# Kernel optimization log

Hardware: AMD Instinct MI355X
Metric: run time of the kernel (lower is better)

Reference implementation:

```python
import jax, jax.numpy as jnp
import numpy as np

N = 30000   # total nodes
E = 240000  # edges
B = 64      # graphs / proteins
H = 10      # GATv2 heads
C = 78      # per-head out dim (= xd_features)
D = H * C   # 780
SEQ = 1000
EMB = 128
LH = 64     # LSTM hidden per direction


def _lstm_dir(xs, Wih, Whh, bih, bhh, reverse):
    # xs: [T, Bn, EMB]; PyTorch gate order i,f,g,o
    Bn = xs.shape[1]
    h0 = jnp.zeros((Bn, LH), xs.dtype)
    def step(carry, xt):
        h, c = carry
        z = xt @ Wih.T + h @ Whh.T + bih + bhh
        i, f, g, o = jnp.split(z, 4, axis=-1)
        c = jax.nn.sigmoid(f) * c + jax.nn.sigmoid(i) * jnp.tanh(g)
        h = jax.nn.sigmoid(o) * jnp.tanh(c)
        return (h, c), h
    _, hs = jax.lax.scan(step, (h0, h0), xs, reverse=reverse)
    return hs


def setup_inputs() -> dict:
    k = jax.random.key(0)
    nxt = lambda i: jax.random.fold_in(k, i)
    s = 0.05
    d = {}
    d['x'] = jax.random.normal(nxt(0), (N, C), jnp.float32)
    d['edge_index'] = jax.random.randint(nxt(1), (2, E), 0, N)
    d['batch'] = jnp.sort(jax.random.randint(nxt(2), (N,), 0, B))
    d['target'] = jax.random.randint(nxt(3), (B, SEQ), 0, 26)
    # GATv2Conv params (share_weights=False)
    d['Wl'] = jax.random.normal(nxt(4), (C, D), jnp.float32) * s
    d['Wr'] = jax.random.normal(nxt(5), (C, D), jnp.float32) * s
    d['att'] = jax.random.normal(nxt(6), (H, C), jnp.float32) * s
    d['gat_b'] = jnp.zeros((D,), jnp.float32)
    # GCNConv params
    d['gcn_w'] = jax.random.normal(nxt(7), (D, D), jnp.float32) * s
    d['gcn_b'] = jnp.zeros((D,), jnp.float32)
    # protein branch
    d['emb'] = jax.random.normal(nxt(8), (26, EMB), jnp.float32) * s
    for tag, base in (('f', 9), ('b', 13)):
        d['Wih_' + tag] = jax.random.normal(nxt(base), (4 * LH, EMB), jnp.float32) * s
        d['Whh_' + tag] = jax.random.normal(nxt(base + 1), (4 * LH, LH), jnp.float32) * s
        d['bih_' + tag] = jnp.zeros((4 * LH,), jnp.float32)
        d['bhh_' + tag] = jnp.zeros((4 * LH,), jnp.float32)
    d['conv_w'] = jax.random.normal(nxt(17), (32, SEQ, 8), jnp.float32) * s
    d['conv_b'] = jnp.zeros((32,), jnp.float32)
    d['fcp_w'] = jax.random.normal(nxt(18), (32 * 121, 128), jnp.float32) * s
    d['fcp_b'] = jnp.zeros((128,), jnp.float32)
    # combined MLP (actual concat dim = 2*780 + 128 = 1688)
    d['fc1_w'] = jax.random.normal(nxt(19), (1688, 1024), jnp.float32) * s
    d['fc1_b'] = jnp.zeros((1024,), jnp.float32)
    d['fc2_w'] = jax.random.normal(nxt(20), (1024, 512), jnp.float32) * s
    d['fc2_b'] = jnp.zeros((512,), jnp.float32)
    d['out_w'] = jax.random.normal(nxt(21), (512, 1), jnp.float32) * s
    d['out_b'] = jnp.zeros((1,), jnp.float32)
    return d


def reference(x, edge_index, batch, target, Wl, Wr, att, gat_b, gcn_w, gcn_b,
              emb, Wih_f, Whh_f, bih_f, bhh_f, Wih_b, Whh_b, bih_b, bhh_b,
              conv_w, conv_b, fcp_w, fcp_b, fc1_w, fc1_b, fc2_w, fc2_b,
              out_w, out_b):
    # ---- graph branch (eval mode: dropout off) ----
    loops = jnp.arange(N)
    src = jnp.concatenate([edge_index[0], loops])  # self loops (PyG default)
    dst = jnp.concatenate([edge_index[1], loops])

    # GATv2Conv
    xl = (x @ Wl).reshape(N, H, C)
    xr = (x @ Wr).reshape(N, H, C)
    e = jax.nn.leaky_relu(xl[src] + xr[dst], 0.2)       # [E+N, H, C]
    logit = jnp.einsum('ehc,hc->eh', e, att)            # [E+N, H]
    m = jax.ops.segment_max(logit, dst, num_segments=N)
    ex = jnp.exp(logit - m[dst])
    den = jax.ops.segment_sum(ex, dst, num_segments=N)
    alpha = ex / den[dst]
    h = jax.ops.segment_sum(alpha[:, :, None] * xl[src], dst, num_segments=N)
    h = jax.nn.elu(h.reshape(N, D) + gat_b)

    # GCNConv with symmetric normalization
    hw = h @ gcn_w
    deg = jax.ops.segment_sum(jnp.ones_like(src, jnp.float32), dst, num_segments=N)
    dinv = jnp.where(deg > 0, jax.lax.rsqrt(jnp.maximum(deg, 1e-12)), 0.0)
    norm = dinv[src] * dinv[dst]
    g = jax.ops.segment_sum(norm[:, None] * hw[src], dst, num_segments=N) + gcn_b
    g = jax.nn.relu(g)

    # global max + mean pooling per graph
    gmax = jax.ops.segment_max(g, batch, num_segments=B)
    cnt = jax.ops.segment_sum(jnp.ones((N,), jnp.float32), batch, num_segments=B)
    gmean = jax.ops.segment_sum(g, batch, num_segments=B) / jnp.maximum(cnt, 1.0)[:, None]
    graph_feat = jnp.concatenate([gmax, gmean], axis=1)  # [B, 1560]

    # ---- protein branch ----
    et = emb[target]                                     # [B, SEQ, EMB]
    # nn.LSTM default batch_first=False: time axis is axis 0 (=B), batch axis is SEQ
    hf = _lstm_dir(et, Wih_f, Whh_f, bih_f, bhh_f, reverse=False)
    hb = _lstm_dir(et, Wih_b, Whh_b, bih_b, bhh_b, reverse=True)
    hcat = jnp.concatenate([hf, hb], axis=-1)            # [B, SEQ, 128]
    conv = jax.lax.conv_general_dilated(hcat, conv_w, (1,), 'VALID',
                                        dimension_numbers=('NCH', 'OIH', 'NCH'))
    conv = conv + conv_b[None, :, None]                  # [B, 32, 121]
    prot = conv.reshape(B, 32 * 121) @ fcp_w + fcp_b     # [B, 128]

    # ---- combined head ----
    comb = jnp.concatenate([graph_feat, prot], axis=1)   # [B, 1688]
    h1 = jax.nn.relu(comb @ fc1_w + fc1_b)
    h2 = jax.nn.relu(h1 @ fc2_w + fc2_b)
    return h2 @ out_w + out_b                            # [B, 1]
```

## Files before the change

kernel.cpp:

```cpp
#include <hip/hip_runtime.h>
#include <hip/hip_bf16.h>
#include <math.h>

static constexpr int NN   = 30000;
static constexpr int EE   = 240000;
static constexpr int ET   = EE + NN;
static constexpr int BB   = 64;
static constexpr int HH   = 10;
static constexpr int CC   = 78;
static constexpr int CCP  = 80;
static constexpr int DD   = HH * CC;
static constexpr int DDP  = HH * CCP;
static constexpr int NNP  = 30080;
static constexpr int KXP  = 96;
static constexpr int NBP  = 896;
static constexpr int SEQ  = 1000;
static constexpr int EMB  = 128;
static constexpr int LH   = 64;
static constexpr int COMBD = 2 * DD + 128;
static constexpr int PCHUNK = 64;
static constexpr int USL  = CCP / 2;
static constexpr size_t SLICE_U = (size_t)NNP * USL;

typedef __attribute__((ext_vector_type(8))) short short8;
typedef __attribute__((ext_vector_type(4))) float f32x4;

__device__ __forceinline__ float bflo(unsigned int u) {
    return __uint_as_float(u << 16);
}
__device__ __forceinline__ float bfhi(unsigned int u) {
    return __uint_as_float(u & 0xffff0000u);
}
__device__ __forceinline__ unsigned int pack2bf(float x, float y) {
    __hip_bfloat16 bx = __float2bfloat16(x), by = __float2bfloat16(y);
    unsigned short ux = *reinterpret_cast<unsigned short*>(&bx);
    unsigned short uy = *reinterpret_cast<unsigned short*>(&by);
    return (unsigned int)ux | ((unsigned int)uy << 16);
}
__device__ __forceinline__ float fast_sigmoid(float x) {
    return __builtin_amdgcn_rcpf(1.f + __expf(-x));
}
__device__ __forceinline__ float fast_tanh(float x) {
    float e = __expf(2.f * x);
    return 1.f - 2.f * __builtin_amdgcn_rcpf(e + 1.f);
}
__device__ __forceinline__ void glds16(const unsigned short* g, unsigned short* l) {
    __builtin_amdgcn_global_load_lds(
        (const __attribute__((address_space(1))) unsigned int*)g,
        (__attribute__((address_space(3))) unsigned int*)l, 16, 0, 0);
}

__global__ __launch_bounds__(256) void gemm_glds_sl(const __hip_bfloat16* __restrict__ A,
                                                    const __hip_bfloat16* __restrict__ Bt,
                                                    __hip_bfloat16* __restrict__ C,
                                                    int M, int N, int Kp) {
    __shared__ unsigned short As[128 * 32];
    __shared__ unsigned short Bs[128 * 32];
    const int tid  = threadIdx.x;
    const int lane = tid & 63, wid = tid >> 6;
    const int wr = wid >> 1, wc = wid & 1;
    const int l15 = lane & 15, l4 = lane >> 4;
    int l = blockIdx.y * gridDim.x + blockIdx.x;
    {
        int nwg = gridDim.x * gridDim.y;
        int q = nwg >> 3, r = nwg & 7;
        int xcd = l & 7, idx = l >> 3;
        l = (xcd < r) ? (xcd * (q + 1) + idx) : (r * (q + 1) + (xcd - r) * q + idx);
    }
    const int bm = (l / gridDim.x) * 128;
    const int bn = (l % gridDim.x) * 128;
    const unsigned short* Au = (const unsigned short*)A;
    const unsigned short* Bu = (const unsigned short*)Bt;
    const int lrow = lane >> 2, lseg = (lane & 3) * 8;

    f32x4 acc[4][4];
#pragma unroll
    for (int m = 0; m < 4; ++m)
#pragma unroll
        for (int n = 0; n < 4; ++n) acc[m][n] = (f32x4){0.f, 0.f, 0.f, 0.f};

    for (int k0 = 0; k0 < Kp; k0 += 32) {
#pragma unroll
        for (int c = 0; c < 2; ++c) {
            int rbase = wid * 32 + c * 16;
            glds16(Au + (size_t)(bm + rbase + lrow) * Kp + k0 + lseg, &As[rbase * 32]);
            glds16(Bu + (size_t)(bn + rbase + lrow) * Kp + k0 + lseg, &Bs[rbase * 32]);
        }
        __syncthreads();
        short8 a[4], b[4];
#pragma unroll
        for (int m = 0; m < 4; ++m)
            a[m] = *reinterpret_cast<const short8*>(&As[(wr * 64 + m * 16 + l15) * 32 + l4 * 8]);
#pragma unroll
        for (int n = 0; n < 4; ++n)
            b[n] = *reinterpret_cast<const short8*>(&Bs[(wc * 64 + n * 16 + l15) * 32 + l4 * 8]);
#pragma unroll
        for (int m = 0; m < 4; ++m)
#pragma unroll
            for (int n = 0; n < 4; ++n)
                acc[m][n] = __builtin_amdgcn_mfma_f32_16x16x32_bf16(a[m], b[n], acc[m][n], 0, 0, 0);
        __syncthreads();
    }
#pragma unroll
    for (int m = 0; m < 4; ++m)
#pragma unroll
        for (int n = 0; n < 4; ++n)
#pragma unroll
            for (int r = 0; r < 4; ++r) {
                int row = bm + wr * 64 + m * 16 + l4 * 4 + r;
                int col = bn + wc * 64 + n * 16 + l15;
                if (row < M && col < N) {
                    int sl = col / CC, c = col % CC;
                    C[(size_t)sl * NNP * CCP + (size_t)row * CCP + c] =
                        __float2bfloat16(acc[m][n][r]);
                }
            }
}

__global__ __launch_bounds__(256) void gemm_bf16_mfma(const __hip_bfloat16* __restrict__ A,
                                                      const __hip_bfloat16* __restrict__ Bt,
                                                      float* __restrict__ C,
                                                      int M, int N, int K, int ldc) {
    constexpr int LDS_S = 40;
    __shared__ unsigned short As[128 * LDS_S];
    __shared__ unsigned short Bs[128 * LDS_S];
    const int tid  = threadIdx.x;
    const int lane = tid & 63, wid = tid >> 6;
    const int wr = wid >> 1, wc = wid & 1;
    const int l15 = lane & 15, l4 = lane >> 4;
    int l = blockIdx.y * gridDim.x + blockIdx.x;
    {
        int nwg = gridDim.x * gridDim.y;
        int q = nwg >> 3, r = nwg & 7;
        int xcd = l & 7, idx = l >> 3;
        l = (xcd < r) ? (xcd * (q + 1) + idx) : (r * (q + 1) + (xcd - r) * q + idx);
    }
    const int bm = (l / gridDim.x) * 128;
    const int bn = (l % gridDim.x) * 128;
    const int tr = tid >> 2, tc = (tid & 3) * 8;

    const unsigned short* Au = (const unsigned short*)A;
    const unsigned short* Bu = (const unsigned short*)Bt;

    f32x4 acc[4][4];
#pragma unroll
    for (int m = 0; m < 4; ++m)
#pragma unroll
        for (int n = 0; n < 4; ++n) acc[m][n] = (f32x4){0.f, 0.f, 0.f, 0.f};

    for (int k0 = 0; k0 < K; k0 += 32) {
#pragma unroll
        for (int half = 0; half < 2; ++half) {
            int row = tr + half * 64;
            {
                int grow = bm + row;
                short8 sv;
                if (grow < M && k0 + tc + 8 <= K) {
                    const unsigned int* p = (const unsigned int*)(Au + (size_t)grow * K + k0 + tc);
#pragma unroll
                    for (int j = 0; j < 4; ++j) {
                        unsigned int u = p[j];
                        sv[2 * j]     = (short)(u & 0xffffu);
                        sv[2 * j + 1] = (short)(u >> 16);
                    }
                } else {
#pragma unroll
                    for (int j = 0; j < 8; ++j) {
                        int gk = k0 + tc + j;
                        sv[j] = (grow < M && gk < K) ? (short)Au[(size_t)grow * K + gk] : (short)0;
                    }
                }
                *reinterpret_cast<short8*>(&As[row * LDS_S + tc]) = sv;
            }
            {
                int grow = bn + row;
                short8 sv;
                if (grow < N && k0 + tc + 8 <= K) {
                    const unsigned int* p = (const unsigned int*)(Bu + (size_t)grow * K + k0 + tc);
#pragma unroll
                    for (int j = 0; j < 4; ++j) {
                        unsigned int u = p[j];
                        sv[2 * j]     = (short)(u & 0xffffu);
                        sv[2 * j + 1] = (short)(u >> 16);
                    }
                } else {
#pragma unroll
                    for (int j = 0; j < 8; ++j) {
                        int gk = k0 + tc + j;
                        sv[j] = (grow < N && gk < K) ? (short)Bu[(size_t)grow * K + gk] : (short)0;
                    }
                }
                *reinterpret_cast<short8*>(&Bs[row * LDS_S + tc]) = sv;
            }
        }
        __syncthreads();
        short8 a[4], b[4];
#pragma unroll
        for (int m = 0; m < 4; ++m)
            a[m] = *reinterpret_cast<const short8*>(&As[(wr * 64 + m * 16 + l15) * LDS_S + l4 * 8]);
#pragma unroll
        for (int n = 0; n < 4; ++n)
            b[n] = *reinterpret_cast<const short8*>(&Bs[(wc * 64 + n * 16 + l15) * LDS_S + l4 * 8]);
#pragma unroll
        for (int m = 0; m < 4; ++m)
#pragma unroll
            for (int n = 0; n < 4; ++n)
                acc[m][n] = __builtin_amdgcn_mfma_f32_16x16x32_bf16(a[m], b[n], acc[m][n], 0, 0, 0);
        __syncthreads();
    }
#pragma unroll
    for (int m = 0; m < 4; ++m)
#pragma unroll
        for (int n = 0; n < 4; ++n)
#pragma unroll
            for (int r = 0; r < 4; ++r) {
                int row = bm + wr * 64 + m * 16 + l4 * 4 + r;
                int col = bn + wc * 64 + n * 16 + l15;
                if (row < M && col < N)
                    C[(size_t)row * ldc + col] = acc[m][n][r];
            }
}

__global__ void pad_x(const float* __restrict__ x, __hip_bfloat16* __restrict__ xp) {
    int idx = blockIdx.x * blockDim.x + threadIdx.x;
    if (idx >= NNP * KXP) return;
    int r = idx / KXP, c = idx % KXP;
    float v = (r < NN && c < CC) ? x[(size_t)r * CC + c] : 0.f;
    xp[idx] = __float2bfloat16(v);
}

__global__ void pad_wT(const float* __restrict__ w, __hip_bfloat16* __restrict__ wt) {
    int idx = blockIdx.x * blockDim.x + threadIdx.x;
    if (idx >= NBP * KXP) return;
    int n = idx / KXP, k = idx % KXP;
    float v = (n < DD && k < CC) ? w[(size_t)k * DD + n] : 0.f;
    wt[idx] = __float2bfloat16(v);
}

__global__ void pad_gcwT(const float* __restrict__ w, __hip_bfloat16* __restrict__ wt) {
    int idx = blockIdx.x * blockDim.x + threadIdx.x;
    if (idx >= NBP * DDP) return;
    int n = idx / DDP, kp = idx % DDP;
    int kc = kp % CCP;
    int k = (kp / CCP) * CC + kc;
    float v = (n < DD && kc < CC) ? w[(size_t)k * DD + n] : 0.f;
    wt[idx] = __float2bfloat16(v);
}

__global__ void transpose_f32(const float* __restrict__ in, float* __restrict__ out,
                              int Kdim, int Ndim) {
    int idx = blockIdx.x * blockDim.x + threadIdx.x;
    if (idx >= Kdim * Ndim) return;
    int n = idx / Kdim, k = idx % Kdim;
    out[idx] = in[(size_t)k * Ndim + n];
}

__global__ void pad_att(const float* __restrict__ att, float* __restrict__ att_p) {
    int idx = blockIdx.x * blockDim.x + threadIdx.x;
    if (idx >= HH * CCP) return;
    int h = idx / CCP, c = idx % CCP;
    att_p[idx] = (c < CC) ? att[h * CC + c] : 0.f;
}

__global__ void zero_pads(unsigned int* __restrict__ a, unsigned int* __restrict__ b) {
    int idx = blockIdx.x * blockDim.x + threadIdx.x;
    if (idx >= NN * HH) return;
    int n = idx / HH, h = idx % HH;
    size_t p = (size_t)h * SLICE_U + (size_t)n * USL + (USL - 1);
    a[p] = 0u;
    b[p] = 0u;
}

template <int ACT>
__global__ __launch_bounds__(256) void gemm_skinny(const float* __restrict__ A,
                                                   const float* __restrict__ Bt,
                                                   const float* __restrict__ bias,
                                                   float* __restrict__ C,
                                                   int M, int N, int K, int ldc) {
    int oidx = blockIdx.x * 4 + (threadIdx.x >> 6);
    int lane = threadIdx.x & 63;
    if (oidx >= M * N) return;
    int row = oidx / N, col = oidx % N;
    const float4* a = (const float4*)(A + (size_t)row * K);
    const float4* b = (const float4*)(Bt + (size_t)col * K);
    int K4 = K >> 2;
    float s = 0.f;
    for (int i = lane; i < K4; i += 64) {
        float4 x = a[i], y = b[i];
        s += x.x * y.x + x.y * y.y + x.z * y.z + x.w * y.w;
    }
#pragma unroll
    for (int off = 32; off; off >>= 1) s += __shfl_xor(s, off);
    if (lane == 0) {
        s += bias[col];
        if (ACT == 1) s = fmaxf(s, 0.f);
        C[(size_t)row * ldc + col] = s;
    }
}

__global__ void deg_count(const int* __restrict__ ei, int* __restrict__ deg) {
    int e = blockIdx.x * blockDim.x + threadIdx.x;
    if (e >= ET) return;
    int d = (e < EE) ? ei[EE + e] : (e - EE);
    atomicAdd(&deg[d], 1);
}

__global__ __launch_bounds__(1024) void scan_kernel(const int* __restrict__ deg,
                                                    int* __restrict__ offs) {
    __shared__ int lds[1024];
    int tid = threadIdx.x;
    const int chunk = (NN + 1023) / 1024;
    int base = tid * chunk;
    int s = 0;
    for (int i = 0; i < chunk; ++i) {
        int idx = base + i;
        if (idx < NN) s += deg[idx];
    }
    lds[tid] = s;
    __syncthreads();
    for (int d = 1; d < 1024; d <<= 1) {
        int v = (tid >= d) ? lds[tid - d] : 0;
        __syncthreads();
        lds[tid] += v;
        __syncthreads();
    }
    int run = (tid == 0) ? 0 : lds[tid - 1];
    for (int i = 0; i < chunk; ++i) {
        int idx = base + i;
        if (idx < NN) { offs[idx] = run; run += deg[idx]; }
    }
    if (tid == 1023) offs[NN] = lds[1023];
}

__global__ void csr_fill(const int* __restrict__ ei, const int* __restrict__ offs,
                         int* __restrict__ cursor, int* __restrict__ csr_src,
                         int* __restrict__ csr_dst) {
    int e = blockIdx.x * blockDim.x + threadIdx.x;
    if (e >= ET) return;
    int s = (e < EE) ? ei[e] : (e - EE);
    int d = (e < EE) ? ei[EE + e] : (e - EE);
    int pos = atomicAdd(&cursor[d], 1);
    int slot = offs[d] + pos;
    csr_src[slot] = s;
    csr_dst[slot] = d;
}

__global__ void dinv_kernel(const int* __restrict__ deg, float* __restrict__ dinv) {
    int n = blockIdx.x * blockDim.x + threadIdx.x;
    if (n >= NN) return;
    float dg = (float)deg[n];
    dinv[n] = (dg > 0.f) ? 1.f / sqrtf(dg) : 0.f;
}

__device__ __forceinline__ float dot2lr(unsigned int a, unsigned int b, float w0, float w1) {
    float v0 = bflo(a) + bflo(b);
    float v1 = bfhi(a) + bfhi(b);
    v0 = (v0 > 0.f) ? v0 : 0.2f * v0;
    v1 = (v1 > 0.f) ? v1 : 0.2f * v1;
    return w0 * v0 + w1 * v1;
}

__global__ void gat_logits(const unsigned short* __restrict__ xl_sl,
                           const unsigned short* __restrict__ xr_sl,
                           const float* __restrict__ att_p, const int* __restrict__ csr_src,
                           const int* __restrict__ csr_dst, float* __restrict__ logit_hm) {
    int i = blockIdx.x * blockDim.x + threadIdx.x;
    int h = blockIdx.y;
    if (i >= ET) return;
    int s = csr_src[i], d = csr_dst[i];
    const uint4* pl = (const uint4*)(xl_sl + (size_t)h * NNP * CCP + (size_t)s * CCP);
    const uint4* pr = (const uint4*)(xr_sl + (size_t)h * NNP * CCP + (size_t)d * CCP);
    const float* pa = att_p + h * CCP;
    float acc = 0.f;
#pragma unroll
    for (int q = 0; q < CCP / 8; ++q) {
        uint4 a = pl[q], b = pr[q];
        const float* p8 = pa + q * 8;
        acc += dot2lr(a.x, b.x, p8[0], p8[1]);
        acc += dot2lr(a.y, b.y, p8[2], p8[3]);
        acc += dot2lr(a.z, b.z, p8[4], p8[5]);
        acc += dot2lr(a.w, b.w, p8[6], p8[7]);
    }
    logit_hm[(size_t)h * ET + i] = acc;
}

__global__ void gat_softmax(const int* __restrict__ offs, float* __restrict__ logit_hm) {
    int idx = blockIdx.x * blockDim.x + threadIdx.x;
    if (idx >= NN * HH) return;
    int n = idx / HH, h = idx % HH;
    int i0 = offs[n], i1 = offs[n + 1];
    float* lg = logit_hm + (size_t)h * ET;
    float m = -1e30f;
    for (int i = i0; i < i1; ++i) m = fmaxf(m, lg[i]);
    float den = 0.f;
    for (int i = i0; i < i1; ++i) {
        float e = __expf(lg[i] - m);
        lg[i] = e;
        den += e;
    }
    float inv = __builtin_amdgcn_rcpf(den);
    for (int i = i0; i < i1; ++i) lg[i] *= inv;
}

__global__ __launch_bounds__(256) void gat_aggregate(const int* __restrict__ offs,
                                                     const int* __restrict__ csr_src,
                                                     const float* __restrict__ alpha_hm,
                                                     const unsigned int* __restrict__ xl_sl,
                                                     const float* __restrict__ gat_b,
                                                     unsigned int* __restrict__ hout) {
    int n = blockIdx.x;
    int tid = threadIdx.x;
    int i0 = offs[n], i1 = offs[n + 1];
    const int U = DDP / 2;
    int u0 = tid, u1 = tid + 256;
    bool v1 = (u1 < U);
    int h0 = u0 / USL, c0 = u0 % USL;
    int h1 = v1 ? u1 / USL : 0, c1 = v1 ? u1 % USL : 0;
    const unsigned int* s0 = xl_sl + (size_t)h0 * SLICE_U + c0;
    const unsigned int* s1 = xl_sl + (size_t)h1 * SLICE_U + c1;
    const float* a0p = alpha_hm + (size_t)h0 * ET;
    const float* a1p = alpha_hm + (size_t)h1 * ET;
    float lo0 = 0.f, hi0 = 0.f, lo1 = 0.f, hi1 = 0.f;
    for (int i = i0; i < i1; ++i) {
        int src = csr_src[i];
        unsigned int w0 = s0[(size_t)src * USL];
        float p0 = a0p[i];
        lo0 += p0 * bflo(w0);
        hi0 += p0 * bfhi(w0);
        if (v1) {
            unsigned int w1 = s1[(size_t)src * USL];
            float p1 = a1p[i];
            lo1 += p1 * bflo(w1);
            hi1 += p1 * bfhi(w1);
        }
    }
    unsigned int ov0 = 0u, ov1 = 0u;
    if (c0 != USL - 1) {
        int d = h0 * CC + 2 * c0;
        float x = lo0 + gat_b[d];     x = (x > 0.f) ? x : __expf(x) - 1.f;
        float y = hi0 + gat_b[d + 1]; y = (y > 0.f) ? y : __expf(y) - 1.f;
        ov0 = pack2bf(x, y);
    }
    hout[(size_t)n * U + u0] = ov0;
    if (v1) {
        if (c1 != USL - 1) {
            int d = h1 * CC + 2 * c1;
            float x = lo1 + gat_b[d];     x = (x > 0.f) ? x : __expf(x) - 1.f;
            float y = hi1 + gat_b[d + 1]; y = (y > 0.f) ? y : __expf(y) - 1.f;
            ov1 = pack2bf(x, y);
        }
        hout[(size_t)n * U + u1] = ov1;
    }
}

__global__ __launch_bounds__(256) void gcn_aggregate(const int* __restrict__ offs,
                                                     const int* __restrict__ csr_src,
                                                     const float* __restrict__ dinv,
                                                     const unsigned int* __restrict__ hw_sl,
                                                     const float* __restrict__ gcn_b,
                                                     unsigned int* __restrict__ g_sl) {
    int n = blockIdx.x;
    int tid = threadIdx.x;
    float din = dinv[n];
    int i0 = offs[n], i1 = offs[n + 1];
    const int U = DDP / 2;
    int u0 = tid, u1 = tid + 256;
    bool v1 = (u1 < U);
    int h0 = u0 / USL, c0 = u0 % USL;
    int h1 = v1 ? u1 / USL : 0, c1 = v1 ? u1 % USL : 0;
    const unsigned int* s0 = hw_sl + (size_t)h0 * SLICE_U + c0;
    const unsigned int* s1 = hw_sl + (size_t)h1 * SLICE_U + c1;
    float lo0 = 0.f, hi0 = 0.f, lo1 = 0.f, hi1 = 0.f;
    for (int i = i0; i < i1; ++i) {
        int src = csr_src[i];
        float w = dinv[src] * din;
        unsigned int w0 = s0[(size_t)src * USL];
        lo0 += w * bflo(w0);
        hi0 += w * bfhi(w0);
        if (v1) {
            unsigned int w1 = s1[(size_t)src * USL];
            lo1 += w * bflo(w1);
            hi1 += w * bfhi(w1);
        }
    }
    if (c0 != USL - 1) {
        int d = h0 * CC + 2 * c0;
        float x = fmaxf(lo0 + gcn_b[d], 0.f);
        float y = fmaxf(hi0 + gcn_b[d + 1], 0.f);
        g_sl[(size_t)h0 * SLICE_U + (size_t)n * USL + c0] = pack2bf(x, y);
    }
    if (v1 && c1 != USL - 1) {
        int d = h1 * CC + 2 * c1;
        float x = fmaxf(lo1 + gcn_b[d], 0.f);
        float y = fmaxf(hi1 + gcn_b[d + 1], 0.f);
        g_sl[(size_t)h1 * SLICE_U + (size_t)n * USL + c1] = pack2bf(x, y);
    }
}

__global__ void graph_ranges(const int* __restrict__ batch, int* __restrict__ gstart,
                             int* __restrict__ gend) {
    int n = blockIdx.x * blockDim.x + threadIdx.x;
    if (n >= NN) return;
    int b = batch[n];
    if (n == 0 || batch[n - 1] != b) gstart[b] = n;
    if (n == NN - 1 || batch[n + 1] != b) gend[b] = n + 1;
}

__global__ __launch_bounds__(256) void pool_partial(const unsigned int* __restrict__ g_sl,
                                                    const int* __restrict__ batch,
                                                    float* __restrict__ pmax,
                                                    float* __restrict__ psum) {
    int chunk0 = blockIdx.x * PCHUNK;
    int tid = threadIdx.x;
    __shared__ int bsh[PCHUNK];
    for (int i = tid; i < PCHUNK; i += 256) {
        int n = chunk0 + i;
        bsh[i] = (n < NN) ? batch[n] : -1;
    }
    __syncthreads();
    const int U = DDP / 2;
    int u0 = tid, u1 = tid + 256;
    bool v1 = (u1 < U);
    int h0 = u0 / USL, c0 = u0 % USL;
    int h1 = v1 ? u1 / USL : 0, c1 = v1 ? u1 % USL : 0;
    const unsigned int* s0 = g_sl + (size_t)h0 * SLICE_U + c0;
    const unsigned int* s1 = g_sl + (size_t)h1 * SLICE_U + c1;
    float mA = 0.f, mB = 0.f, mC = 0.f, mD = 0.f;
    float sA = 0.f, sB = 0.f, sC = 0.f, sD = 0.f;
    int curb = bsh[0];
    auto flush = [&](int b) {
        if (b >= 0) {
            if (c0 != USL - 1) {
                int d = h0 * CC + 2 * c0;
                atomicMax((unsigned int*)&pmax[(size_t)b * DD + d], __float_as_uint(mA));
                atomicAdd(&psum[(size_t)b * DD + d], sA);
                atomicMax((unsigned int*)&pmax[(size_t)b * DD + d + 1], __float_as_uint(mB));
                atomicAdd(&psum[(size_t)b * DD + d + 1], sB);
            }
            if (v1 && c1 != USL - 1) {
                int d = h1 * CC + 2 * c1;
                atomicMax((unsigned int*)&pmax[(size_t)b * DD + d], __float_as_uint(mC));
                atomicAdd(&psum[(size_t)b * DD + d], sC);
                atomicMax((unsigned int*)&pmax[(size_t)b * DD + d + 1], __float_as_uint(mD));
                atomicAdd(&psum[(size_t)b * DD + d + 1], sD);
            }
        }
        mA = mB = mC = mD = 0.f;
        sA = sB = sC = sD = 0.f;
    };
    for (int i = 0; i < PCHUNK; ++i) {
        int n = chunk0 + i;
        if (n >= NN) break;
        int b = bsh[i];
        if (b != curb) { flush(curb); curb = b; }
        unsigned int w0 = s0[(size_t)n * USL];
        float x = bflo(w0), y = bfhi(w0);
        mA = fmaxf(mA, x); sA += x;
        mB = fmaxf(mB, y); sB += y;
        if (v1) {
            unsigned int w1 = s1[(size_t)n * USL];
            float z = bflo(w1), t = bfhi(w1);
            mC = fmaxf(mC, z); sC += z;
            mD = fmaxf(mD, t); sD += t;
        }
    }
    flush(curb);
}

__global__ void pool_finalize(const float* __restrict__ pmax, const float* __restrict__ psum,
                              const int* __restrict__ gstart, const int* __restrict__ gend,
                              float* __restrict__ comb) {
    int idx = blockIdx.x * blockDim.x + threadIdx.x;
    if (idx >= BB * DD) return;
    int b = idx / DD, d = idx % DD;
    float cnt = fmaxf((float)(gend[b] - gstart[b]), 1.f);
    comb[(size_t)b * COMBD + d] = pmax[idx];
    comb[(size_t)b * COMBD + DD + d] = psum[idx] / cnt;
}

__global__ void proj26_kernel(const float* __restrict__ emb,
                              const float* __restrict__ Wih_f, const float* __restrict__ bih_f,
                              const float* __restrict__ bhh_f,
                              const float* __restrict__ Wih_b, const float* __restrict__ bih_b,
                              const float* __restrict__ bhh_b, float* __restrict__ proj) {
    int dir = blockIdx.x, row = blockIdx.y, j = threadIdx.x;
    const float* W = dir ? Wih_b : Wih_f;
    const float* b1 = dir ? bih_b : bih_f;
    const float* b2 = dir ? bhh_b : bhh_f;
    float acc = b1[j] + b2[j];
    const float* e = emb + row * EMB;
    const float* w = W + j * EMB;
    for (int k = 0; k < EMB; ++k) acc += e[k] * w[k];
    proj[(dir * 26 + row) * 256 + j] = acc;
}

__global__ __launch_bounds__(256) void lstm_kernel(const int* __restrict__ target,
                                                   const float* __restrict__ proj26,
                                                   const float* __restrict__ Whh_f,
                                                   const float* __restrict__ Whh_b,
                                                   float* __restrict__ hcat) {
    int n = blockIdx.x;
    int dir = blockIdx.y;
    int tid = threadIdx.x;
    const float* Whh = dir ? Whh_b : Whh_f;
    const float* proj = proj26 + dir * 26 * 256;
    const int gate = tid >> 6;
    float w[LH];
#pragma unroll
    for (int u4 = 0; u4 < LH / 4; ++u4) {
        float4 v = *reinterpret_cast<const float4*>(Whh + tid * LH + u4 * 4);
        w[u4 * 4 + 0] = v.x; w[u4 * 4 + 1] = v.y;
        w[u4 * 4 + 2] = v.z; w[u4 * 4 + 3] = v.w;
    }
    __shared__ float h_lds[LH];
    __shared__ float z_lds[256];
    __shared__ int tgt_lds[BB];
    float c_reg = 0.f;
    if (tid < LH) h_lds[tid] = 0.f;
    if (tid < BB) {
        int t = dir ? (BB - 1 - tid) : tid;
        tgt_lds[tid] = target[t * SEQ + n];
    }
    __syncthreads();
    float pnext = proj[tgt_lds[0] * 256 + tid];
    for (int s = 0; s < BB; ++s) {
        float a0 = 0.f, a1 = 0.f, a2 = 0.f, a3 = 0.f;
#pragma unroll
        for (int u = 0; u < LH; u += 4) {
            float4 hv = *reinterpret_cast<const float4*>(&h_lds[u]);
            a0 += w[u] * hv.x;
            a1 += w[u + 1] * hv.y;
            a2 += w[u + 2] * hv.z;
            a3 += w[u + 3] * hv.w;
        }
        float z = pnext + a0 + a1 + a2 + a3;
        if (s + 1 < BB) pnext = proj[tgt_lds[s + 1] * 256 + tid];
        z_lds[tid] = (gate == 2) ? fast_tanh(z) : fast_sigmoid(z);
        __syncthreads();
        if (tid < LH) {
            float ig = z_lds[tid];
            float fg = z_lds[LH + tid];
            float gg = z_lds[2 * LH + tid];
            float og = z_lds[3 * LH + tid];
            float c = fg * c_reg + ig * gg;
            float h = og * fast_tanh(c);
            c_reg = c;
            h_lds[tid] = h;
            int t = dir ? (BB - 1 - s) : s;
            hcat[((size_t)t * SEQ + n) * 128 + dir * LH + tid] = h;
        }
        __syncthreads();
    }
}

__global__ __launch_bounds__(256) void transpose_hcat(const float* __restrict__ hcat,
                                                      unsigned short* __restrict__ hcatT) {
    int b = blockIdx.z;
    int i0 = blockIdx.y * 32;
    int h0 = blockIdx.x * 32;
    int th = threadIdx.x & 31;
    int ti = threadIdx.x >> 5;
    __shared__ float t[32][33];
#pragma unroll
    for (int r = 0; r < 4; ++r) {
        int i = i0 + ti + r * 8;
        if (i < SEQ) t[ti + r * 8][th] = hcat[((size_t)b * SEQ + i) * 128 + h0 + th];
    }
    __syncthreads();
#pragma unroll
    for (int r = 0; r < 4; ++r) {
        int h = h0 + ti + r * 8;
        int i = i0 + th;
        if (i < SEQ) {
            unsigned int u = __float_as_uint(t[th][ti + r * 8]);
            unsigned int lsb = (u >> 16) & 1u;
            u += 0x7fffu + lsb;
            hcatT[((size_t)b * 128 + h) * SEQ + i] = (unsigned short)(u >> 16);
        }
    }
}

__global__ void reshape_convw(const float* __restrict__ conv_w, __hip_bfloat16* __restrict__ wT) {
    int idx = blockIdx.x * blockDim.x + threadIdx.x;
    if (idx >= 256 * SEQ) return;
    int np = idx / SEQ, i = idx % SEQ;
    int o = np >> 3, k = np & 7;
    wT[idx] = __float2bfloat16(conv_w[((size_t)o * SEQ + i) * 8 + k]);
}

__global__ void conv_finalize(const float* __restrict__ T, const float* __restrict__ conv_b,
                              float* __restrict__ convout) {
    int idx = blockIdx.x * blockDim.x + threadIdx.x;
    if (idx >= BB * 32 * 121) return;
    int p = idx % 121;
    int o = (idx / 121) % 32;
    int b = idx / (121 * 32);
    float acc = conv_b[o];
#pragma unroll
    for (int k = 0; k < 8; ++k)
        acc += T[(size_t)(b * 128 + p + k) * 256 + o * 8 + k];
    convout[(size_t)b * 3872 + o * 121 + p] = acc;
}

extern "C" void kernel_launch(void* const* d_in, const int* in_sizes, int n_in,
                              void* d_out, int out_size, void* d_ws, size_t ws_size,
                              hipStream_t stream) {
    const float* x      = (const float*)d_in[0];
    const int*   ei     = (const int*)d_in[1];
    const int*   batch  = (const int*)d_in[2];
    const int*   target = (const int*)d_in[3];
    const float* Wl     = (const float*)d_in[4];
    const float* Wr     = (const float*)d_in[5];
    const float* att    = (const float*)d_in[6];
    const float* gat_b  = (const float*)d_in[7];
    const float* gcn_w  = (const float*)d_in[8];
    const float* gcn_b  = (const float*)d_in[9];
    const float* emb    = (const float*)d_in[10];
    const float* Wih_f  = (const float*)d_in[11];
    const float* Whh_f  = (const float*)d_in[12];
    const float* bih_f  = (const float*)d_in[13];
    const float* bhh_f  = (const float*)d_in[14];
    const float* Wih_b  = (const float*)d_in[15];
    const float* Whh_b  = (const float*)d_in[16];
    const float* bih_b  = (const float*)d_in[17];
    const float* bhh_b  = (const float*)d_in[18];
    const float* conv_w = (const float*)d_in[19];
    const float* conv_b = (const float*)d_in[20];
    const float* fcp_w  = (const float*)d_in[21];
    const float* fcp_b  = (const float*)d_in[22];
    const float* fc1_w  = (const float*)d_in[23];
    const float* fc1_b  = (const float*)d_in[24];
    const float* fc2_w  = (const float*)d_in[25];
    const float* fc2_b  = (const float*)d_in[26];
    const float* out_w  = (const float*)d_in[27];
    const float* out_b  = (const float*)d_in[28];
    float* out = (float*)d_out;
    (void)n_in; (void)in_sizes; (void)out_size;

    char* ws = (char*)d_ws;
    size_t o = 0;
    auto alloc = [&](size_t bytes) {
        char* p = ws + o;
        o = (o + bytes + 255) & ~(size_t)255;
        return p;
    };
    constexpr size_t HALF = (size_t)HH * NNP * CCP * 2;
    char* region = (char*)alloc(2 * HALF);
    __hip_bfloat16* xl_sl = (__hip_bfloat16*)region;
    __hip_bfloat16* xr_sl = (__hip_bfloat16*)(region + HALF);
    __hip_bfloat16* hw_sl = (__hip_bfloat16*)region;
    __hip_bfloat16* g_sl  = (__hip_bfloat16*)(region + HALF);
    char* rp = region;
    auto palloc = [&](size_t bytes) {
        char* p = rp;
        rp += (bytes + 255) & ~(size_t)255;
        return p;
    };
    float* hcat    = (float*)palloc((size_t)BB * SEQ * 128 * 4);
    float* proj26  = (float*)palloc(2 * 26 * 256 * 4);
    float* convout = (float*)palloc((size_t)BB * 3872 * 4);
    __hip_bfloat16* wT = (__hip_bfloat16*)palloc((size_t)256 * SEQ * 2);
    unsigned short* hcatT = (unsigned short*)palloc((size_t)BB * 128 * SEQ * 2);
    float* T = (float*)palloc((size_t)BB * 128 * 256 * 4);
    __hip_bfloat16* h_bf  = (__hip_bfloat16*)alloc((size_t)NNP * DDP * 2);
    __hip_bfloat16* x_bf  = (__hip_bfloat16*)alloc((size_t)NNP * KXP * 2);
    __hip_bfloat16* wl_t  = (__hip_bfloat16*)alloc((size_t)NBP * KXP * 2);
    __hip_bfloat16* wr_t  = (__hip_bfloat16*)alloc((size_t)NBP * KXP * 2);
    __hip_bfloat16* gcw_t = (__hip_bfloat16*)alloc((size_t)NBP * DDP * 2);
    float* att_p  = (float*)alloc((size_t)HH * CCP * 4);
    float* fcp_wt = (float*)alloc((size_t)3872 * 128 * 4);
    float* fc1_wt = (float*)alloc((size_t)COMBD * 1024 * 4);
    float* fc2_wt = (float*)alloc((size_t)1024 * 512 * 4);
    float* out_wt = (float*)alloc((size_t)512 * 4);
    float* logit    = (float*)alloc((size_t)ET * HH * 4);
    int*   csr_src  = (int*)alloc((size_t)ET * 4);
    int*   csr_dst  = (int*)alloc((size_t)ET * 4);
    int*   deg      = (int*)alloc((size_t)NN * 4);
    int*   cursor   = (int*)alloc((size_t)NN * 4);
    int*   offs     = (int*)alloc((size_t)(NN + 1) * 4);
    float* dinv     = (float*)alloc((size_t)NN * 4);
    int*   gstart   = (int*)alloc(64 * 4);
    int*   gend     = (int*)alloc(64 * 4);
    float* pmax     = (float*)alloc((size_t)BB * DD * 4);
    float* psum     = (float*)alloc((size_t)BB * DD * 4);
    float* comb     = (float*)alloc((size_t)BB * COMBD * 4);
    float* h1       = (float*)alloc((size_t)BB * 1024 * 4);
    float* h2       = (float*)alloc((size_t)BB * 512 * 4);
    if (o > ws_size) return;

    hipMemsetAsync(deg, 0, (size_t)NN * 4, stream);
    hipMemsetAsync(cursor, 0, (size_t)NN * 4, stream);
    hipMemsetAsync(gstart, 0, 64 * 4, stream);
    hipMemsetAsync(gend, 0, 64 * 4, stream);
    hipMemsetAsync(pmax, 0, (size_t)BB * DD * 4, stream);
    hipMemsetAsync(psum, 0, (size_t)BB * DD * 4, stream);

    {
        dim3 grid(2, 26);
        proj26_kernel<<<grid, 256, 0, stream>>>(emb, Wih_f, bih_f, bhh_f, Wih_b, bih_b, bhh_b, proj26);
    }
    {
        dim3 grid(SEQ, 2);
        lstm_kernel<<<grid, 256, 0, stream>>>(target, proj26, Whh_f, Whh_b, hcat);
    }
    {
        dim3 grid(4, 32, BB);
        transpose_hcat<<<grid, 256, 0, stream>>>(hcat, hcatT);
    }
    reshape_convw<<<(256 * SEQ + 255) / 256, 256, 0, stream>>>(conv_w, wT);
    {
        dim3 grid(2, 64);
        gemm_bf16_mfma<<<grid, 256, 0, stream>>>((const __hip_bfloat16*)hcatT, wT, T,
                                                 BB * 128, 256, SEQ, 256);
    }
    conv_finalize<<<(BB * 32 * 121 + 255) / 256, 256, 0, stream>>>(T, conv_b, convout);
    transpose_f32<<<(3872 * 128 + 255) / 256, 256, 0, stream>>>(fcp_w, fcp_wt, 3872, 128);
    gemm_skinny<0><<<(BB * 128 + 3) / 4, 256, 0, stream>>>(convout, fcp_wt, fcp_b,
                                                           comb + 2 * DD, BB, 128, 3872, COMBD);

    pad_x<<<(NNP * KXP + 255) / 256, 256, 0, stream>>>(x, x_bf);
    pad_wT<<<(NBP * KXP + 255) / 256, 256, 0, stream>>>(Wl, wl_t);
    pad_wT<<<(NBP * KXP + 255) / 256, 256, 0, stream>>>(Wr, wr_t);
    pad_gcwT<<<(NBP * DDP + 255) / 256, 256, 0, stream>>>(gcn_w, gcw_t);
    pad_att<<<(HH * CCP + 255) / 256, 256, 0, stream>>>(att, att_p);
    transpose_f32<<<(COMBD * 1024 + 255) / 256, 256, 0, stream>>>(fc1_w, fc1_wt, COMBD, 1024);
    transpose_f32<<<(1024 * 512 + 255) / 256, 256, 0, stream>>>(fc2_w, fc2_wt, 1024, 512);
    transpose_f32<<<(512 + 255) / 256, 256, 0, stream>>>(out_w, out_wt, 512, 1);

    dim3 ggrid((DD + 127) / 128, NNP / 128);
    gemm_glds_sl<<<ggrid, 256, 0, stream>>>(x_bf, wl_t, xl_sl, NN, DD, KXP);
    gemm_glds_sl<<<ggrid, 256, 0, stream>>>(x_bf, wr_t, xr_sl, NN, DD, KXP);
    zero_pads<<<(NN * HH + 255) / 256, 256, 0, stream>>>((unsigned int*)xl_sl, (unsigned int*)xr_sl);
    deg_count<<<(ET + 255) / 256, 256, 0, stream>>>(ei, deg);
    scan_kernel<<<1, 1024, 0, stream>>>(deg, offs);
    csr_fill<<<(ET + 255) / 256, 256, 0, stream>>>(ei, offs, cursor, csr_src, csr_dst);
    dinv_kernel<<<(NN + 255) / 256, 256, 0, stream>>>(deg, dinv);
    {
        dim3 grid((ET + 255) / 256, HH);
        gat_logits<<<grid, 256, 0, stream>>>((const unsigned short*)xl_sl,
                                             (const unsigned short*)xr_sl,
                                             att_p, csr_src, csr_dst, logit);
    }
    gat_softmax<<<(NN * HH + 255) / 256, 256, 0, stream>>>(offs, logit);
    gat_aggregate<<<NN, 256, 0, stream>>>(offs, csr_src, logit,
                                          (const unsigned int*)xl_sl, gat_b,
                                          (unsigned int*)h_bf);
    {
        dim3 g2((DD + 127) / 128, NNP / 128);
        gemm_glds_sl<<<g2, 256, 0, stream>>>(h_bf, gcw_t, hw_sl, NN, DD, DDP);
    }
    gcn_aggregate<<<NN, 256, 0, stream>>>(offs, csr_src, dinv,
                                          (const unsigned int*)hw_sl, gcn_b,
                                          (unsigned int*)g_sl);
    graph_ranges<<<(NN + 255) / 256, 256, 0, stream>>>(batch, gstart, gend);
    pool_partial<<<(NN + PCHUNK - 1) / PCHUNK, 256, 0, stream>>>((const unsigned int*)g_sl,
                                                                 batch, pmax, psum);
    pool_finalize<<<(BB * DD + 255) / 256, 256, 0, stream>>>(pmax, psum, gstart, gend, comb);

    gemm_skinny<1><<<(BB * 1024 + 3) / 4, 256, 0, stream>>>(comb, fc1_wt, fc1_b, h1,
                                                            BB, 1024, COMBD, 1024);
    gemm_skinny<1><<<(BB * 512 + 3) / 4, 256, 0, stream>>>(h1, fc2_wt, fc2_b, h2,
                                                           BB, 512, 1024, 512);
    gemm_skinny<0><<<(BB + 3) / 4, 256, 0, stream>>>(h2, out_wt, out_b, out,
                                                     BB, 1, 512, 1);
}
```

Measured before the change: 864.4 us.

## Remove second barrier in LSTM step via redundant per-wave cell update

Each of the four wavefronts now computes the cell and hidden update redundantly into its own private copy of h in LDS, and the gate buffer is double-buffered by step parity. This removes the second __syncthreads per timestep, leaving one barrier per step on the serial recurrence. The cost is four times the cell-update work and extra LDS, and it relies on each wave reading only the h copy it wrote itself.

```diff
diff --git a/kernel.cpp b/kernel.cpp
--- a/kernel.cpp
+++ b/kernel.cpp
@@ -602,9 +602,10 @@
     int n = blockIdx.x;
     int dir = blockIdx.y;
     int tid = threadIdx.x;
+    const int lane = tid & 63;
+    const int wid = tid >> 6;
     const float* Whh = dir ? Whh_b : Whh_f;
     const float* proj = proj26 + dir * 26 * 256;
-    const int gate = tid >> 6;
     float w[LH];
 #pragma unroll
     for (int u4 = 0; u4 < LH / 4; ++u4) {
@@ -612,11 +613,11 @@
         w[u4 * 4 + 0] = v.x; w[u4 * 4 + 1] = v.y;
         w[u4 * 4 + 2] = v.z; w[u4 * 4 + 3] = v.w;
     }
-    __shared__ float h_lds[LH];
-    __shared__ float z_lds[256];
+    __shared__ float h_lds[4][LH];
+    __shared__ float z_lds[2][256];
     __shared__ int tgt_lds[BB];
     float c_reg = 0.f;
-    if (tid < LH) h_lds[tid] = 0.f;
+    h_lds[wid][lane] = 0.f;
     if (tid < BB) {
         int t = dir ? (BB - 1 - tid) : tid;
         tgt_lds[tid] = target[t * SEQ + n];
@@ -624,10 +625,11 @@
     __syncthreads();
     float pnext = proj[tgt_lds[0] * 256 + tid];
     for (int s = 0; s < BB; ++s) {
+        const float* hme = h_lds[wid];
         float a0 = 0.f, a1 = 0.f, a2 = 0.f, a3 = 0.f;
 #pragma unroll
         for (int u = 0; u < LH; u += 4) {
-            float4 hv = *reinterpret_cast<const float4*>(&h_lds[u]);
+            float4 hv = *reinterpret_cast<const float4*>(&hme[u]);
             a0 += w[u] * hv.x;
             a1 += w[u + 1] * hv.y;
             a2 += w[u + 2] * hv.z;
@@ -635,21 +637,21 @@
         }
         float z = pnext + a0 + a1 + a2 + a3;
         if (s + 1 < BB) pnext = proj[tgt_lds[s + 1] * 256 + tid];
-        z_lds[tid] = (gate == 2) ? fast_tanh(z) : fast_sigmoid(z);
+        z_lds[s & 1][tid] = (wid == 2) ? fast_tanh(z) : fast_sigmoid(z);
         __syncthreads();
-        if (tid < LH) {
-            float ig = z_lds[tid];
-            float fg = z_lds[LH + tid];
-            float gg = z_lds[2 * LH + tid];
-            float og = z_lds[3 * LH + tid];
-            float c = fg * c_reg + ig * gg;
-            float h = og * fast_tanh(c);
-            c_reg = c;
-            h_lds[tid] = h;
+        const float* zb = z_lds[s & 1];
+        float ig = zb[lane];
+        float fg = zb[LH + lane];
+        float gg = zb[2 * LH + lane];
+        float og = zb[3 * LH + lane];
+        float c = fg * c_reg + ig * gg;
+        float h = og * fast_tanh(c);
+        c_reg = c;
+        h_lds[wid][lane] = h;
+        if (wid == 0) {
             int t = dir ? (BB - 1 - s) : s;
-            hcat[((size_t)t * SEQ + n) * 128 + dir * LH + tid] = h;
-        }
-        __syncthreads();
+            hcat[((size_t)t * SEQ + n) * 128 + dir * LH + lane] = h;
+        }
     }
 }
 
```

New measurement: 868.4 us. About the same (+0.5%).
